# Kernel optimization log

Measured on AMD Instinct MI355X. Metric: run time of the kernel, lower is better.

Reference implementation:

```python
import jax, jax.numpy as jnp
import numpy as np

N = 50000
E = 1600000
IN_CH = 128
OUT_CH = 128
NEG_SLOPE = 0.2


def _gat_conv(x, W, att_src, att_dst, bias, src, dst, heads, out_ch, concat):
    # x: [N, F_in], W: [F_in, heads*out_ch], att_*: [heads, out_ch]
    n = x.shape[0]
    h = (x @ W).reshape(n, heads, out_ch)                    # [N, H, C]
    a_src = jnp.einsum('nhc,hc->nh', h, att_src)             # [N, H]
    a_dst = jnp.einsum('nhc,hc->nh', h, att_dst)             # [N, H]
    logits = jax.nn.leaky_relu(a_src[src] + a_dst[dst], NEG_SLOPE)  # [Etot, H]
    m = jax.ops.segment_max(logits, dst, num_segments=n)     # per-dst max (self-loops ensure non-empty)
    e = jnp.exp(logits - m[dst])
    denom = jax.ops.segment_sum(e, dst, num_segments=n)
    alpha = e / denom[dst]                                   # [Etot, H]
    msgs = h[src] * alpha[:, :, None]                        # [Etot, H, C]
    out = jax.ops.segment_sum(msgs, dst, num_segments=n)     # [N, H, C]
    out = out.reshape(n, heads * out_ch) if concat else out.mean(axis=1)
    return out + bias


def setup_inputs() -> dict:
    key = jax.random.key(0)
    ks = jax.random.split(key, 12)
    x = jax.random.normal(ks[0], (N, IN_CH), dtype=jnp.float32)
    edge_index = jax.random.randint(ks[1], (2, E), 0, N, dtype=jnp.int32)
    s = 0.1
    W_map = jax.random.normal(ks[2], (IN_CH, OUT_CH), dtype=jnp.float32) * s
    b_map = jnp.zeros((OUT_CH,), dtype=jnp.float32)
    # conv1: 128 -> 8 per head, 8 heads
    W1 = jax.random.normal(ks[3], (OUT_CH, 64), dtype=jnp.float32) * s
    att_src1 = jax.random.normal(ks[4], (8, 8), dtype=jnp.float32) * s
    att_dst1 = jax.random.normal(ks[5], (8, 8), dtype=jnp.float32) * s
    b1 = jnp.zeros((64,), dtype=jnp.float32)
    # conv2: 64 -> 128, 1 head, concat=False
    W2 = jax.random.normal(ks[6], (64, OUT_CH), dtype=jnp.float32) * s
    att_src2 = jax.random.normal(ks[7], (1, OUT_CH), dtype=jnp.float32) * s
    att_dst2 = jax.random.normal(ks[8], (1, OUT_CH), dtype=jnp.float32) * s
    b2 = jnp.zeros((OUT_CH,), dtype=jnp.float32)
    return {"x": x, "edge_index": edge_index, "W_map": W_map, "b_map": b_map,
            "W1": W1, "att_src1": att_src1, "att_dst1": att_dst1, "b1": b1,
            "W2": W2, "att_src2": att_src2, "att_dst2": att_dst2, "b2": b2}


def reference(x, edge_index, W_map, b_map, W1, att_src1, att_dst1, b1,
              W2, att_src2, att_dst2, b2):
    # add self-loops (PyG GATConv default)
    loops = jnp.arange(N, dtype=edge_index.dtype)
    src = jnp.concatenate([edge_index[0], loops])
    dst = jnp.concatenate([edge_index[1], loops])
    h = x @ W_map + b_map                                   # feature_mapping (dropout inactive in eval)
    h = _gat_conv(h, W1, att_src1, att_dst1, b1, src, dst, heads=8, out_ch=8, concat=True)
    h = jax.nn.elu(h)
    out = _gat_conv(h, W2, att_src2, att_dst2, b2, src, dst, heads=1, out_ch=OUT_CH, concat=False)
    return out
```

## Files before the change

### kernel.cpp

```cpp
#include <hip/hip_runtime.h>
#include <cstdint>
#include <cstddef>

#define NEG_SLOPE 0.2f
#define NBIN_MAX 1024
#define CAP_T 2560

typedef __attribute__((ext_vector_type(8))) short bf16x8;
typedef __attribute__((ext_vector_type(4))) float f32x4;

__device__ __forceinline__ float leaky(float x) { return x > 0.f ? x : NEG_SLOPE * x; }
__device__ __forceinline__ float blo(unsigned u) { return __uint_as_float(u << 16); }
__device__ __forceinline__ float bhi(unsigned u) { return __uint_as_float(u & 0xffff0000u); }
__device__ __forceinline__ unsigned short f2b(float f) {
    unsigned b = __float_as_uint(f);
    return (unsigned short)((b + 0x7fffu + ((b >> 16) & 1u)) >> 16);
}

__global__ void prep_kernel(const float* __restrict__ Wm, const float* __restrict__ W1,
                            const float* __restrict__ bm, const float* __restrict__ W2,
                            unsigned short* __restrict__ WcT, float* __restrict__ bc,
                            unsigned short* __restrict__ W2T, int* __restrict__ ccur,
                            int nbin) {
    int t = blockIdx.x * 256 + threadIdx.x;
    if (t < nbin) ccur[t] = 0;
    if (t < 8192) {
        int n = t >> 7, k = t & 127;
        float acc = 0.f;
        for (int c = 0; c < 128; c++) acc = fmaf(Wm[k * 128 + c], W1[c * 64 + n], acc);
        WcT[n * 128 + k] = f2b(acc);
        if (t < 64) {
            float a = 0.f;
            for (int c = 0; c < 128; c++) a = fmaf(bm[c], W1[c * 64 + t], a);
            bc[t] = a;
        }
    } else if (t < 16384) {
        int u = t - 8192;
        int n = u >> 6, k = u & 63;
        W2T[n * 64 + k] = f2b(W2[k * 128 + n]);
    }
}

__global__ __launch_bounds__(256) void gemm1_mfma(
    const float* __restrict__ x, const unsigned short* __restrict__ WcT,
    const float* __restrict__ bc, const float* __restrict__ att_s,
    const float* __restrict__ att_d, unsigned short* __restrict__ h1b,
    float* __restrict__ as1, float* __restrict__ ad1, int N) {
    int wave = threadIdx.x >> 6, l = threadIdx.x & 63;
    int mtile = blockIdx.x * 4 + wave;
    int mtiles = N >> 4;
    if (mtile >= mtiles) return;
    int lm = l & 15, quad = l >> 4;
    const float* xr = x + ((size_t)(mtile * 16 + lm)) * 128 + quad * 8;
    f32x4 acc[4];
#pragma unroll
    for (int nt = 0; nt < 4; nt++) acc[nt] = (f32x4){0.f, 0.f, 0.f, 0.f};
#pragma unroll
    for (int kk = 0; kk < 4; kk++) {
        float4 xa = ((const float4*)(xr + kk * 32))[0];
        float4 xb = ((const float4*)(xr + kk * 32 + 4))[0];
        bf16x8 a;
        a[0] = (short)f2b(xa.x); a[1] = (short)f2b(xa.y);
        a[2] = (short)f2b(xa.z); a[3] = (short)f2b(xa.w);
        a[4] = (short)f2b(xb.x); a[5] = (short)f2b(xb.y);
        a[6] = (short)f2b(xb.z); a[7] = (short)f2b(xb.w);
#pragma unroll
        for (int nt = 0; nt < 4; nt++) {
            bf16x8 b = *(const bf16x8*)(WcT + (nt * 16 + lm) * 128 + kk * 32 + quad * 8);
            acc[nt] = __builtin_amdgcn_mfma_f32_16x16x32_bf16(a, b, acc[nt], 0, 0, 0);
        }
    }
    float vs[4][4], vd[4][4];
#pragma unroll
    for (int nt = 0; nt < 4; nt++) {
        int col = nt * 16 + lm;
        float sA = att_s[col], dA = att_d[col], bcv = bc[col];
#pragma unroll
        for (int r = 0; r < 4; r++) {
            float hv = acc[nt][r] + bcv;
            int row = mtile * 16 + quad * 4 + r;
            h1b[(size_t)row * 64 + col] = f2b(hv);
            vs[nt][r] = hv * sA;
            vd[nt][r] = hv * dA;
        }
    }
#pragma unroll
    for (int m = 1; m < 8; m <<= 1)
#pragma unroll
        for (int nt = 0; nt < 4; nt++)
#pragma unroll
            for (int r = 0; r < 4; r++) {
                vs[nt][r] += __shfl_xor(vs[nt][r], m);
                vd[nt][r] += __shfl_xor(vd[nt][r], m);
            }
    if ((lm & 7) == 0) {
        int hbase = lm >> 3;
#pragma unroll
        for (int nt = 0; nt < 4; nt++) {
            int H = 2 * nt + hbase;
#pragma unroll
            for (int r = 0; r < 4; r++) {
                int row = mtile * 16 + quad * 4 + r;
                as1[row * 8 + H] = vs[nt][r];
                ad1[row * 8 + H] = vd[nt][r];
            }
        }
    }
}

__global__ __launch_bounds__(256) void scatter2_kernel(
    const int* __restrict__ src, const int* __restrict__ dst, int E, int nbin,
    int* __restrict__ ccur, unsigned* __restrict__ tmp) {
    __shared__ int cnt[NBIN_MAX];
    for (int i = threadIdx.x; i < nbin; i += 256) cnt[i] = 0;
    __syncthreads();
    int E4 = E >> 2;
    int chunk4 = (E4 + gridDim.x - 1) / gridDim.x;
    int b4 = blockIdx.x * chunk4;
    int e4 = b4 + chunk4; if (e4 > E4) e4 = E4;
    const int4* dst4 = (const int4*)dst;
    const int4* src4 = (const int4*)src;
    bool last = (blockIdx.x == gridDim.x - 1);
    for (int i = b4 + threadIdx.x; i < e4; i += 256) {
        int4 d = dst4[i];
        atomicAdd(&cnt[d.x >> 6], 1);
        atomicAdd(&cnt[d.y >> 6], 1);
        atomicAdd(&cnt[d.z >> 6], 1);
        atomicAdd(&cnt[d.w >> 6], 1);
    }
    if (last)
        for (int i = (E4 << 2) + threadIdx.x; i < E; i += 256)
            atomicAdd(&cnt[dst[i] >> 6], 1);
    __syncthreads();
    for (int i = threadIdx.x; i < nbin; i += 256) {
        int c = cnt[i];
        cnt[i] = c ? atomicAdd(&ccur[i], c) : 0;
    }
    __syncthreads();
    for (int i = b4 + threadIdx.x; i < e4; i += 256) {
        int4 d = dst4[i];
        int4 s = src4[i];
#pragma unroll
        for (int k = 0; k < 4; k++) {
            int dd = (k == 0) ? d.x : (k == 1) ? d.y : (k == 2) ? d.z : d.w;
            int ss = (k == 0) ? s.x : (k == 1) ? s.y : (k == 2) ? s.z : s.w;
            int bin = dd >> 6;
            int p = atomicAdd(&cnt[bin], 1);
            if (p < CAP_T)
                tmp[(size_t)bin * CAP_T + p] = ((unsigned)ss << 6) | (unsigned)(dd & 63);
        }
    }
    if (last)
        for (int i = (E4 << 2) + threadIdx.x; i < E; i += 256) {
            int dd = dst[i];
            int bin = dd >> 6;
            int p = atomicAdd(&cnt[bin], 1);
            if (p < CAP_T)
                tmp[(size_t)bin * CAP_T + p] = ((unsigned)src[i] << 6) | (unsigned)(dd & 63);
        }
}

__global__ __launch_bounds__(256) void bin_finalize(
    const unsigned* __restrict__ tmp, const int* __restrict__ ccur,
    int* __restrict__ off, int* __restrict__ degv,
    unsigned short* __restrict__ bucket, int N) {
    __shared__ int cnt[64];
    __shared__ int cur[64];
    int tid = threadIdx.x, b = blockIdx.x;
    if (tid < 64) cnt[tid] = 0;
    __syncthreads();
    int ecnt = ccur[b]; if (ecnt > CAP_T) ecnt = CAP_T;
    const unsigned* t = tmp + (size_t)b * CAP_T;
    for (int i = tid; i < ecnt; i += 256)
        atomicAdd(&cnt[t[i] & 63u], 1);
    __syncthreads();
    if (tid < 64) {
        int v = cnt[tid];
        int incl = v;
#pragma unroll
        for (int s = 1; s < 64; s <<= 1) {
            int u = __shfl_up(incl, s);
            if (tid >= s) incl += u;
        }
        int base = b * CAP_T + (incl - v);
        int node = b * 64 + tid;
        if (node < N) { off[node] = base; degv[node] = v; }
        cur[tid] = base;
    }
    __syncthreads();
    for (int i = tid; i < ecnt; i += 256) {
        unsigned u = t[i];
        int p = atomicAdd(&cur[u & 63u], 1);
        bucket[p] = (unsigned short)(u >> 6);
    }
}

__global__ __launch_bounds__(256) void conv1_agg(
    const int* __restrict__ off, const int* __restrict__ degv,
    const unsigned short* __restrict__ bucket,
    const unsigned* __restrict__ h1b, const float* __restrict__ as1,
    const float* __restrict__ ad1, const float* __restrict__ b1,
    unsigned* __restrict__ h1act, int N) {
    __shared__ uint2 lw[4][32][8];
    int wave = threadIdx.x >> 6, l = threadIdx.x & 63;
    int n = blockIdx.x * 4 + wave;
    if (n >= N) return;
    int begin = off[n];
    int deg = degv[n];
    int h = l & 7, eslot = l >> 3;
    float adst_h = ad1[n * 8 + h];
    float wself_h = __expf(leaky(as1[n * 8 + h] + adst_h));
    int c = l & 31, hp = c >> 2, half = l >> 5;
    float wself_c = __shfl(wself_h, hp);
    float acc0 = 0.f, acc1 = 0.f;
    if (half == 0) {
        unsigned u = h1b[(size_t)n * 32 + c];
        acc0 = wself_c * blo(u);
        acc1 = wself_c * bhi(u);
    }
    float den_l = 0.f;
    unsigned ps[4]; float pa[4];
#pragma unroll
    for (int k = 0; k < 4; k++) {
        int j = eslot + 8 * k;
        ps[k] = (j < deg) ? (unsigned)bucket[begin + j] : 0u;
    }
#pragma unroll
    for (int k = 0; k < 4; k++) pa[k] = as1[ps[k] * 8 + h];
    for (int c0 = 0; c0 < deg; c0 += 32) {
#pragma unroll
        for (int k = 0; k < 4; k++) {
            int e = eslot + 8 * k;
            float w = __expf(leaky(pa[k] + adst_h));
            if (c0 + e >= deg) w = 0.f;
            den_l += w;
            lw[wave][e][h] = make_uint2(__float_as_uint(w), ps[k]);
        }
        int c1 = c0 + 32;
        if (c1 < deg) {
#pragma unroll
            for (int k = 0; k < 4; k++) {
                int j = c1 + eslot + 8 * k;
                ps[k] = (j < deg) ? (unsigned)bucket[begin + j] : 0u;
            }
#pragma unroll
            for (int k = 0; k < 4; k++) pa[k] = as1[ps[k] * 8 + h];
        }
        int cend = deg - c0; if (cend > 32) cend = 32;
        int e = half;
        for (; e + 14 < cend; e += 16) {
            float w[8]; unsigned s[8], u[8];
#pragma unroll
            for (int k = 0; k < 8; k++) {
                uint2 p = lw[wave][e + 2 * k][hp];
                w[k] = __uint_as_float(p.x); s[k] = p.y;
            }
#pragma unroll
            for (int k = 0; k < 8; k++) u[k] = h1b[(size_t)s[k] * 32 + c];
#pragma unroll
            for (int k = 0; k < 8; k++) {
                acc0 = fmaf(w[k], blo(u[k]), acc0);
                acc1 = fmaf(w[k], bhi(u[k]), acc1);
            }
        }
        for (; e < cend; e += 2) {
            uint2 p = lw[wave][e][hp];
            unsigned u = h1b[(size_t)p.y * 32 + c];
            float w = __uint_as_float(p.x);
            acc0 = fmaf(w, blo(u), acc0);
            acc1 = fmaf(w, bhi(u), acc1);
        }
    }
    den_l += __shfl_xor(den_l, 8);
    den_l += __shfl_xor(den_l, 16);
    den_l += __shfl_xor(den_l, 32);
    float den_full = den_l + wself_h;
    float den_c = __shfl(den_full, hp);
    acc0 += __shfl_xor(acc0, 32);
    acc1 += __shfl_xor(acc1, 32);
    if (half == 0) {
        float inv = 1.f / den_c;
        float2 bb = ((const float2*)b1)[c];
        float o0 = acc0 * inv + bb.x;
        float o1 = acc1 * inv + bb.y;
        o0 = o0 > 0.f ? o0 : __expf(o0) - 1.f;
        o1 = o1 > 0.f ? o1 : __expf(o1) - 1.f;
        h1act[(size_t)n * 32 + c] = (unsigned)f2b(o0) | ((unsigned)f2b(o1) << 16);
    }
}

__global__ __launch_bounds__(256) void gemm2_mfma(
    const unsigned short* __restrict__ h1act, const unsigned short* __restrict__ W2T,
    const float* __restrict__ att_s2, const float* __restrict__ att_d2,
    unsigned short* __restrict__ h2b, float* __restrict__ as2, float* __restrict__ ad2,
    int N) {
    int wave = threadIdx.x >> 6, l = threadIdx.x & 63;
    int mtile = blockIdx.x * 4 + wave;
    int mtiles = N >> 4;
    if (mtile >= mtiles) return;
    int lm = l & 15, quad = l >> 4;
    const unsigned short* ar = h1act + (size_t)(mtile * 16 + lm) * 64 + quad * 8;
    bf16x8 a0 = *(const bf16x8*)(ar);
    bf16x8 a1 = *(const bf16x8*)(ar + 32);
    f32x4 acc[8];
#pragma unroll
    for (int nt = 0; nt < 8; nt++) acc[nt] = (f32x4){0.f, 0.f, 0.f, 0.f};
#pragma unroll
    for (int nt = 0; nt < 8; nt++) {
        const unsigned short* br = W2T + (nt * 16 + lm) * 64 + quad * 8;
        bf16x8 b0 = *(const bf16x8*)(br);
        bf16x8 b1v = *(const bf16x8*)(br + 32);
        acc[nt] = __builtin_amdgcn_mfma_f32_16x16x32_bf16(a0, b0, acc[nt], 0, 0, 0);
        acc[nt] = __builtin_amdgcn_mfma_f32_16x16x32_bf16(a1, b1v, acc[nt], 0, 0, 0);
    }
    float vs[4] = {0.f, 0.f, 0.f, 0.f}, vd[4] = {0.f, 0.f, 0.f, 0.f};
#pragma unroll
    for (int nt = 0; nt < 8; nt++) {
        int col = nt * 16 + lm;
        float sA = att_s2[col], dA = att_d2[col];
#pragma unroll
        for (int r = 0; r < 4; r++) {
            float hv = acc[nt][r];
            int row = mtile * 16 + quad * 4 + r;
            h2b[(size_t)row * 128 + col] = f2b(hv);
            vs[r] = fmaf(hv, sA, vs[r]);
            vd[r] = fmaf(hv, dA, vd[r]);
        }
    }
#pragma unroll
    for (int m = 1; m < 16; m <<= 1)
#pragma unroll
        for (int r = 0; r < 4; r++) {
            vs[r] += __shfl_xor(vs[r], m);
            vd[r] += __shfl_xor(vd[r], m);
        }
    if (lm == 0) {
#pragma unroll
        for (int r = 0; r < 4; r++) {
            int row = mtile * 16 + quad * 4 + r;
            as2[row] = vs[r];
            ad2[row] = vd[r];
        }
    }
}

__global__ __launch_bounds__(256) void conv2_agg(
    const int* __restrict__ off, const int* __restrict__ degv,
    const unsigned short* __restrict__ bucket,
    const unsigned* __restrict__ h2b, const float* __restrict__ as2,
    const float* __restrict__ ad2, const float* __restrict__ b2,
    float* __restrict__ out, int N) {
    __shared__ uint2 ew[4][64];
    int wave = threadIdx.x >> 6, l = threadIdx.x & 63;
    int n = blockIdx.x * 4 + wave;
    if (n >= N) return;
    int begin = off[n];
    int deg = degv[n];
    float adst = ad2[n];
    float wself = __expf(leaky(as2[n] + adst));
    unsigned us = h2b[(size_t)n * 64 + l];
    float acc0 = wself * blo(us);
    float acc1 = wself * bhi(us);
    float den_l = 0.f;
    for (int c0 = 0; c0 < deg; c0 += 64) {
        int j = c0 + l;
        float w = 0.f; unsigned s = 0;
        if (j < deg) {
            s = bucket[begin + j];
            w = __expf(leaky(as2[s] + adst));
        }
        den_l += w;
        ew[wave][l] = make_uint2(__float_as_uint(w), s);
        int cend = deg - c0; if (cend > 64) cend = 64;
        int jj = 0;
        for (; jj + 8 <= cend; jj += 8) {
            float w[8]; unsigned s8[8], u[8];
#pragma unroll
            for (int k = 0; k < 8; k++) {
                uint2 p = ew[wave][jj + k];
                w[k] = __uint_as_float(p.x); s8[k] = p.y;
            }
#pragma unroll
            for (int k = 0; k < 8; k++) u[k] = h2b[(size_t)s8[k] * 64 + l];
#pragma unroll
            for (int k = 0; k < 8; k++) {
                acc0 = fmaf(w[k], blo(u[k]), acc0);
                acc1 = fmaf(w[k], bhi(u[k]), acc1);
            }
        }
        for (; jj < cend; jj++) {
            uint2 p0 = ew[wave][jj];
            unsigned u0 = h2b[(size_t)p0.y * 64 + l];
            float w0 = __uint_as_float(p0.x);
            acc0 = fmaf(w0, blo(u0), acc0); acc1 = fmaf(w0, bhi(u0), acc1);
        }
    }
#pragma unroll
    for (int s = 1; s < 64; s <<= 1) den_l += __shfl_xor(den_l, s);
    float inv = 1.f / (den_l + wself);
    float2 bb = ((const float2*)b2)[l];
    ((float2*)out)[(size_t)n * 64 + l] =
        make_float2(acc0 * inv + bb.x, acc1 * inv + bb.y);
}

extern "C" void kernel_launch(void* const* d_in, const int* in_sizes, int n_in,
                              void* d_out, int out_size, void* d_ws, size_t ws_size,
                              hipStream_t stream) {
    const float* x   = (const float*)d_in[0];
    const int*   ei  = (const int*)d_in[1];
    const float* Wm  = (const float*)d_in[2];
    const float* bm  = (const float*)d_in[3];
    const float* W1  = (const float*)d_in[4];
    const float* As1 = (const float*)d_in[5];
    const float* Ad1 = (const float*)d_in[6];
    const float* b1  = (const float*)d_in[7];
    const float* W2  = (const float*)d_in[8];
    const float* As2 = (const float*)d_in[9];
    const float* Ad2 = (const float*)d_in[10];
    const float* b2  = (const float*)d_in[11];
    int N = in_sizes[0] / 128;
    int E = in_sizes[1] / 2;
    const int* srcv = ei;
    const int* dstv = ei + E;

    char* p = (char*)d_ws;
    auto alloc = [&](size_t bytes) {
        void* r = (void*)p;
        p += (bytes + 255) & ~(size_t)255;
        return r;
    };
    int nbin = (N + 63) / 64;
    int*   degv   = (int*)alloc((size_t)N * 4);
    int*   off    = (int*)alloc((size_t)N * 4);
    int*   ccur   = (int*)alloc((size_t)nbin * 4);
    unsigned short* bucket = (unsigned short*)alloc((size_t)nbin * CAP_T * 2);
    unsigned short* WcT  = (unsigned short*)alloc(64 * 128 * 2);
    float*          bc   = (float*)alloc(64 * 4);
    unsigned short* W2T  = (unsigned short*)alloc(128 * 64 * 2);
    unsigned short* h1b  = (unsigned short*)alloc((size_t)N * 64 * 2);
    float* a_s1   = (float*)alloc((size_t)N * 8 * 4);
    float* a_d1   = (float*)alloc((size_t)N * 8 * 4);
    unsigned* h1act = (unsigned*)alloc((size_t)N * 64 * 2);
    unsigned short* h2b = (unsigned short*)alloc((size_t)N * 128 * 2);
    unsigned* tmp = (unsigned*)h2b;
    float* a_s2   = (float*)alloc((size_t)N * 4);
    float* a_d2   = (float*)alloc((size_t)N * 4);
    float* outp   = (float*)d_out;

    prep_kernel<<<64, 256, 0, stream>>>(Wm, W1, bm, W2, WcT, bc, W2T, ccur, nbin);
    scatter2_kernel<<<256, 256, 0, stream>>>(srcv, dstv, E, nbin, ccur, tmp);
    gemm1_mfma<<<(N / 16 + 3) / 4, 256, 0, stream>>>(x, WcT, bc, As1, Ad1, h1b, a_s1, a_d1, N);
    bin_finalize<<<nbin, 256, 0, stream>>>(tmp, ccur, off, degv, bucket, N);
    conv1_agg<<<(N + 3) / 4, 256, 0, stream>>>(off, degv, bucket, (const unsigned*)h1b, a_s1, a_d1, b1, h1act, N);
    gemm2_mfma<<<(N / 16 + 3) / 4, 256, 0, stream>>>((const unsigned short*)h1act, W2T, As2, Ad2, h2b, a_s2, a_d2, N);
    conv2_agg<<<(N + 3) / 4, 256, 0, stream>>>(off, degv, bucket, (const unsigned*)h2b, a_s2, a_d2, b2, outp, N);
}
```

Before: 268.5 us.

## Fuse edge scatter with first GEMM and stage bin finalize in LDS

Merges the edge binning scatter and the first MFMA GEMM into one launch, with the first 512 blocks doing the scatter and the rest doing GEMM tiles. The two independent stages can then overlap on the GPU, and one launch is saved. The scatter also moves from 256 to 512 blocks. bin_finalize now reads tmp as uint4, builds each bin's sorted bucket in shared memory, and writes it out with coalesced 16-byte stores instead of scattered 2-byte global writes. The risks are extra LDS per block in bin_finalize and register pressure in the fused kernel, which may lower occupancy for the GEMM part.

```diff
diff --git a/kernel.cpp b/kernel.cpp
--- a/kernel.cpp
+++ b/kernel.cpp
@@ -5,6 +5,7 @@
 #define NEG_SLOPE 0.2f
 #define NBIN_MAX 1024
 #define CAP_T 2560
+#define SC_BLOCKS 512
 
 typedef __attribute__((ext_vector_type(8))) short bf16x8;
 typedef __attribute__((ext_vector_type(4))) float f32x4;
@@ -41,13 +42,65 @@
     }
 }
 
-__global__ __launch_bounds__(256) void gemm1_mfma(
+__global__ __launch_bounds__(256) void phase2_kernel(
+    const int* __restrict__ src, const int* __restrict__ dst, int E, int nbin,
+    int* __restrict__ ccur, unsigned* __restrict__ tmp,
     const float* __restrict__ x, const unsigned short* __restrict__ WcT,
     const float* __restrict__ bc, const float* __restrict__ att_s,
     const float* __restrict__ att_d, unsigned short* __restrict__ h1b,
     float* __restrict__ as1, float* __restrict__ ad1, int N) {
+    __shared__ int cnt[NBIN_MAX];
+    if (blockIdx.x < SC_BLOCKS) {
+        for (int i = threadIdx.x; i < nbin; i += 256) cnt[i] = 0;
+        __syncthreads();
+        int E4 = E >> 2;
+        int chunk4 = (E4 + SC_BLOCKS - 1) / SC_BLOCKS;
+        int b4 = blockIdx.x * chunk4;
+        int e4 = b4 + chunk4; if (e4 > E4) e4 = E4;
+        const int4* dst4 = (const int4*)dst;
+        const int4* src4 = (const int4*)src;
+        bool last = (blockIdx.x == SC_BLOCKS - 1);
+        for (int i = b4 + threadIdx.x; i < e4; i += 256) {
+            int4 d = dst4[i];
+            atomicAdd(&cnt[d.x >> 6], 1);
+            atomicAdd(&cnt[d.y >> 6], 1);
+            atomicAdd(&cnt[d.z >> 6], 1);
+            atomicAdd(&cnt[d.w >> 6], 1);
+        }
+        if (last)
+            for (int i = (E4 << 2) + threadIdx.x; i < E; i += 256)
+                atomicAdd(&cnt[dst[i] >> 6], 1);
+        __syncthreads();
+        for (int i = threadIdx.x; i < nbin; i += 256) {
+            int c = cnt[i];
+            cnt[i] = c ? atomicAdd(&ccur[i], c) : 0;
+        }
+        __syncthreads();
+        for (int i = b4 + threadIdx.x; i < e4; i += 256) {
+            int4 d = dst4[i];
+            int4 s = src4[i];
+#pragma unroll
+            for (int k = 0; k < 4; k++) {
+                int dd = (k == 0) ? d.x : (k == 1) ? d.y : (k == 2) ? d.z : d.w;
+                int ss = (k == 0) ? s.x : (k == 1) ? s.y : (k == 2) ? s.z : s.w;
+                int bin = dd >> 6;
+                int p = atomicAdd(&cnt[bin], 1);
+                if (p < CAP_T)
+                    tmp[(size_t)bin * CAP_T + p] = ((unsigned)ss << 6) | (unsigned)(dd & 63);
+            }
+        }
+        if (last)
+            for (int i = (E4 << 2) + threadIdx.x; i < E; i += 256) {
+                int dd = dst[i];
+                int bin = dd >> 6;
+                int p = atomicAdd(&cnt[bin], 1);
+                if (p < CAP_T)
+                    tmp[(size_t)bin * CAP_T + p] = ((unsigned)src[i] << 6) | (unsigned)(dd & 63);
+            }
+        return;
+    }
     int wave = threadIdx.x >> 6, l = threadIdx.x & 63;
-    int mtile = blockIdx.x * 4 + wave;
+    int mtile = (blockIdx.x - SC_BLOCKS) * 4 + wave;
     int mtiles = N >> 4;
     if (mtile >= mtiles) return;
     int lm = l & 15, quad = l >> 4;
@@ -108,70 +161,28 @@
     }
 }
 
-__global__ __launch_bounds__(256) void scatter2_kernel(
-    const int* __restrict__ src, const int* __restrict__ dst, int E, int nbin,
-    int* __restrict__ ccur, unsigned* __restrict__ tmp) {
-    __shared__ int cnt[NBIN_MAX];
-    for (int i = threadIdx.x; i < nbin; i += 256) cnt[i] = 0;
-    __syncthreads();
-    int E4 = E >> 2;
-    int chunk4 = (E4 + gridDim.x - 1) / gridDim.x;
-    int b4 = blockIdx.x * chunk4;
-    int e4 = b4 + chunk4; if (e4 > E4) e4 = E4;
-    const int4* dst4 = (const int4*)dst;
-    const int4* src4 = (const int4*)src;
-    bool last = (blockIdx.x == gridDim.x - 1);
-    for (int i = b4 + threadIdx.x; i < e4; i += 256) {
-        int4 d = dst4[i];
-        atomicAdd(&cnt[d.x >> 6], 1);
-        atomicAdd(&cnt[d.y >> 6], 1);
-        atomicAdd(&cnt[d.z >> 6], 1);
-        atomicAdd(&cnt[d.w >> 6], 1);
-    }
-    if (last)
-        for (int i = (E4 << 2) + threadIdx.x; i < E; i += 256)
-            atomicAdd(&cnt[dst[i] >> 6], 1);
-    __syncthreads();
-    for (int i = threadIdx.x; i < nbin; i += 256) {
-        int c = cnt[i];
-        cnt[i] = c ? atomicAdd(&ccur[i], c) : 0;
-    }
-    __syncthreads();
-    for (int i = b4 + threadIdx.x; i < e4; i += 256) {
-        int4 d = dst4[i];
-        int4 s = src4[i];
-#pragma unroll
-        for (int k = 0; k < 4; k++) {
-            int dd = (k == 0) ? d.x : (k == 1) ? d.y : (k == 2) ? d.z : d.w;
-            int ss = (k == 0) ? s.x : (k == 1) ? s.y : (k == 2) ? s.z : s.w;
-            int bin = dd >> 6;
-            int p = atomicAdd(&cnt[bin], 1);
-            if (p < CAP_T)
-                tmp[(size_t)bin * CAP_T + p] = ((unsigned)ss << 6) | (unsigned)(dd & 63);
-        }
-    }
-    if (last)
-        for (int i = (E4 << 2) + threadIdx.x; i < E; i += 256) {
-            int dd = dst[i];
-            int bin = dd >> 6;
-            int p = atomicAdd(&cnt[bin], 1);
-            if (p < CAP_T)
-                tmp[(size_t)bin * CAP_T + p] = ((unsigned)src[i] << 6) | (unsigned)(dd & 63);
-        }
-}
-
 __global__ __launch_bounds__(256) void bin_finalize(
     const unsigned* __restrict__ tmp, const int* __restrict__ ccur,
     int* __restrict__ off, int* __restrict__ degv,
     unsigned short* __restrict__ bucket, int N) {
     __shared__ int cnt[64];
     __shared__ int cur[64];
+    __shared__ unsigned short lbkt[CAP_T];
     int tid = threadIdx.x, b = blockIdx.x;
     if (tid < 64) cnt[tid] = 0;
     __syncthreads();
     int ecnt = ccur[b]; if (ecnt > CAP_T) ecnt = CAP_T;
     const unsigned* t = tmp + (size_t)b * CAP_T;
-    for (int i = tid; i < ecnt; i += 256)
+    const uint4* t4 = (const uint4*)t;
+    int e4 = ecnt >> 2;
+    for (int i = tid; i < e4; i += 256) {
+        uint4 v = t4[i];
+        atomicAdd(&cnt[v.x & 63u], 1);
+        atomicAdd(&cnt[v.y & 63u], 1);
+        atomicAdd(&cnt[v.z & 63u], 1);
+        atomicAdd(&cnt[v.w & 63u], 1);
+    }
+    for (int i = (e4 << 2) + tid; i < ecnt; i += 256)
         atomicAdd(&cnt[t[i] & 63u], 1);
     __syncthreads();
     if (tid < 64) {
@@ -182,17 +193,31 @@
             int u = __shfl_up(incl, s);
             if (tid >= s) incl += u;
         }
-        int base = b * CAP_T + (incl - v);
+        int excl = incl - v;
         int node = b * 64 + tid;
-        if (node < N) { off[node] = base; degv[node] = v; }
-        cur[tid] = base;
+        if (node < N) { off[node] = b * CAP_T + excl; degv[node] = v; }
+        cur[tid] = excl;
     }
     __syncthreads();
-    for (int i = tid; i < ecnt; i += 256) {
+    for (int i = tid; i < e4; i += 256) {
+        uint4 v = t4[i];
+        int p0 = atomicAdd(&cur[v.x & 63u], 1); lbkt[p0] = (unsigned short)(v.x >> 6);
+        int p1 = atomicAdd(&cur[v.y & 63u], 1); lbkt[p1] = (unsigned short)(v.y >> 6);
+        int p2 = atomicAdd(&cur[v.z & 63u], 1); lbkt[p2] = (unsigned short)(v.z >> 6);
+        int p3 = atomicAdd(&cur[v.w & 63u], 1); lbkt[p3] = (unsigned short)(v.w >> 6);
+    }
+    for (int i = (e4 << 2) + tid; i < ecnt; i += 256) {
         unsigned u = t[i];
         int p = atomicAdd(&cur[u & 63u], 1);
-        bucket[p] = (unsigned short)(u >> 6);
-    }
+        lbkt[p] = (unsigned short)(u >> 6);
+    }
+    __syncthreads();
+    unsigned short* db = bucket + (size_t)b * CAP_T;
+    int e8 = ecnt >> 3;
+    uint4* d4 = (uint4*)db;
+    const uint4* l4 = (const uint4*)lbkt;
+    for (int i = tid; i < e8; i += 256) d4[i] = l4[i];
+    for (int i = (e8 << 3) + tid; i < ecnt; i += 256) db[i] = lbkt[i];
 }
 
 __global__ __launch_bounds__(256) void conv1_agg(
@@ -447,11 +472,13 @@
     float* a_d2   = (float*)alloc((size_t)N * 4);
     float* outp   = (float*)d_out;
 
+    int mtiles = N >> 4;
+    int gemm_blocks = (mtiles + 3) / 4;
     prep_kernel<<<64, 256, 0, stream>>>(Wm, W1, bm, W2, WcT, bc, W2T, ccur, nbin);
-    scatter2_kernel<<<256, 256, 0, stream>>>(srcv, dstv, E, nbin, ccur, tmp);
-    gemm1_mfma<<<(N / 16 + 3) / 4, 256, 0, stream>>>(x, WcT, bc, As1, Ad1, h1b, a_s1, a_d1, N);
+    phase2_kernel<<<SC_BLOCKS + gemm_blocks, 256, 0, stream>>>(
+        srcv, dstv, E, nbin, ccur, tmp, x, WcT, bc, As1, Ad1, h1b, a_s1, a_d1, N);
     bin_finalize<<<nbin, 256, 0, stream>>>(tmp, ccur, off, degv, bucket, N);
     conv1_agg<<<(N + 3) / 4, 256, 0, stream>>>(off, degv, bucket, (const unsigned*)h1b, a_s1, a_d1, b1, h1act, N);
-    gemm2_mfma<<<(N / 16 + 3) / 4, 256, 0, stream>>>((const unsigned short*)h1act, W2T, As2, Ad2, h2b, a_s2, a_d2, N);
+    gemm2_mfma<<<(mtiles + 3) / 4, 256, 0, stream>>>((const unsigned short*)h1act, W2T, As2, Ad2, h2b, a_s2, a_d2, N);
     conv2_agg<<<(N + 3) / 4, 256, 0, stream>>>(off, degv, bucket, (const unsigned*)h2b, a_s2, a_d2, b2, outp, N);
 }
```

Result: no change. 263.7 us (-1.8%).
